# Optimization experiments

Measured on AMD Instinct MI355X. Metric: run time of the kernel, lower is better.

The kernel has to match this reference:

```python
import jax, jax.numpy as jnp
import numpy as np

K_SIM_SCHEDULE = [4, 8, 16]
K_CON_SCHEDULE = [2, 4, 8]
NEG = 1000000000.0


def _dual_adjacency(h, k_sim, k_con):
    """Binary causal dual adjacency (similar / dissimilar), no gradient."""
    B, T, D = h.shape
    h = jax.lax.stop_gradient(h)
    xn = h / jnp.maximum(jnp.linalg.norm(h, axis=-1, keepdims=True), 1e-12)
    sim = jnp.einsum('btd,bsd->bts', xn, xn)                 # (B,T,T)
    past = jnp.tril(jnp.ones((T, T), h.dtype), -1)           # strictly-past mask
    sim = sim * past - NEG * (1.0 - past)
    eff_sim = min(k_sim, T - 1)
    eff_con = min(k_con, max(0, T - 1 - eff_sim))
    bI = jnp.arange(B)[:, None, None]
    tI = jnp.arange(T)[None, :, None]
    A_sim = jnp.zeros((B, T, T), h.dtype)
    if eff_sim > 0:
        _, top_idx = jax.lax.top_k(sim, eff_sim)             # (B,T,k)
        A_sim = A_sim.at[bI, tI, top_idx].set(1.0) * past
    A_con = jnp.zeros((B, T, T), h.dtype)
    if eff_con > 0:
        sim_con = jnp.where(A_sim > 0, NEG, sim)
        _, bot_idx = jax.lax.top_k(-sim_con, eff_con)        # smallest eff_con
        A_con = A_con.at[bI, tI, bot_idx].set(1.0) * past * (1.0 - A_sim)
    return A_sim, A_con


def _aggregate(h, A):
    # unweighted mean over selected neighbors; empty rows -> zeros
    deg = jnp.sum(A, axis=-1, keepdims=True)
    return jnp.einsum('bts,bsd->btd', A, h) / jnp.maximum(deg, 1.0)


def setup_inputs() -> dict:
    key = jax.random.key(0)
    ks = jax.random.split(key, 2)
    B, T, D, R = 4, 2048, 512, 3
    x = jax.random.normal(ks[0], (B, T, D), dtype=jnp.float32)
    gain = jnp.ones((R, D), dtype=jnp.float32)
    bias = jnp.zeros((R, D), dtype=jnp.float32)
    log_mix = jnp.zeros((R,), dtype=jnp.float32)
    log_alpha = jnp.zeros((R,), dtype=jnp.float32)
    log_momentum = jnp.asarray(1.0, dtype=jnp.float32)
    log_scale = jnp.asarray(0.0, dtype=jnp.float32)
    return {"x": x, "gain": gain, "bias": bias, "log_mix": log_mix,
            "log_alpha": log_alpha, "log_momentum": log_momentum,
            "log_scale": log_scale}


def reference(x, gain, bias, log_mix, log_alpha, log_momentum, log_scale):
    momentum = jax.nn.sigmoid(log_momentum)
    scale = jax.nn.softplus(log_scale) + 0.01
    h = x
    for r in range(len(K_SIM_SCHEDULE)):
        mix = jax.nn.sigmoid(log_mix[r])
        alpha = jax.nn.sigmoid(log_alpha[r])
        A_sim, A_con = _dual_adjacency(h, K_SIM_SCHEDULE[r], K_CON_SCHEDULE[r])
        msg_pos = _aggregate(h, A_sim)
        msg_neg = _aggregate(h, A_con)
        ctx = alpha * msg_pos + (1.0 - alpha) * msg_neg
        blended = mix * h + (1.0 - mix) * ctx
        h_new = jax.nn.gelu(blended * gain[r] + bias[r], approximate=False)
        h = momentum * h + (1.0 - momentum) * h_new
    return (h - x) * scale
```

## Files before the change

kernel.cpp:

```cpp
#include <hip/hip_runtime.h>
#include <hip/hip_bf16.h>
#include <cstdint>
#include <cstddef>

#define BB 4
#define TT 2048
#define DD 512
#define NEG_INF (-3.402823466e+38f)
#define POS_INF (3.402823466e+38f)

typedef __attribute__((ext_vector_type(8))) short bf16x8;
typedef __attribute__((ext_vector_type(8))) unsigned short ushort8;
typedef __attribute__((ext_vector_type(4))) float f32x4;

__device__ __forceinline__ float sigmoidf_(float x){ return 1.0f/(1.0f+expf(-x)); }

__device__ __forceinline__ unsigned short f2bf(float x){
  __hip_bfloat16 b = __float2bfloat16(x);
  return *reinterpret_cast<unsigned short*>(&b);
}

__device__ __forceinline__ unsigned int fwd_map(float f){
  unsigned int b = __float_as_uint(f);
  return b ^ ((b & 0x80000000u) ? 0xFFFFFFFFu : 0x80000000u);
}
__device__ __forceinline__ float inv_map(unsigned int u){
  unsigned int b = (u & 0x80000000u) ? (u ^ 0x80000000u) : ~u;
  return __uint_as_float(b);
}

__global__ __launch_bounds__(64) void k_normsplit(const float* __restrict__ h, float* __restrict__ rnorm,
                                                  unsigned short* __restrict__ Xh, unsigned short* __restrict__ Xl){
  int row = blockIdx.x;
  const float* hr = h + (size_t)row*DD;
  int lane = threadIdx.x;
  float4 v0 = *(const float4*)&hr[lane*4];
  float4 v1 = *(const float4*)&hr[lane*4 + 256];
  float ss = v0.x*v0.x+v0.y*v0.y+v0.z*v0.z+v0.w*v0.w
           + v1.x*v1.x+v1.y*v1.y+v1.z*v1.z+v1.w*v1.w;
  #pragma unroll
  for (int off=32; off; off>>=1) ss += __shfl_xor(ss, off);
  float rn = 1.0f / fmaxf(sqrtf(ss), 1e-12f);
  if (lane==0) rnorm[row] = rn;

  float xs[8] = {v0.x,v0.y,v0.z,v0.w,v1.x,v1.y,v1.z,v1.w};
  unsigned short hb[8], lb[8];
  #pragma unroll
  for (int q=0;q<8;q++){
    float xn = xs[q]*rn;
    unsigned short hh = f2bf(xn);
    __hip_bfloat16 bh = *reinterpret_cast<__hip_bfloat16*>(&hh);
    float rem = xn - __bfloat162float(bh);
    hb[q] = hh; lb[q] = f2bf(rem);
  }
  ushort4 h0 = {hb[0],hb[1],hb[2],hb[3]}, h1 = {hb[4],hb[5],hb[6],hb[7]};
  ushort4 l0 = {lb[0],lb[1],lb[2],lb[3]}, l1 = {lb[4],lb[5],lb[6],lb[7]};
  *(ushort4*)&Xh[(size_t)row*DD + lane*4]       = h0;
  *(ushort4*)&Xh[(size_t)row*DD + lane*4 + 256] = h1;
  *(ushort4*)&Xl[(size_t)row*DD + lane*4]       = l0;
  *(ushort4*)&Xl[(size_t)row*DD + lane*4 + 256] = l1;
}

__global__ __launch_bounds__(256) void k_sim(const unsigned short* __restrict__ Xh,
                                             const unsigned short* __restrict__ Xl,
                                             float* __restrict__ sim, int b0){
  int p = blockIdx.x;
  int jt = (int)((sqrtf(8.0f*(float)p + 1.0f) - 1.0f)*0.5f);
  while ((jt+1)*(jt+2)/2 <= p) jt++;
  while (jt*(jt+1)/2 > p) jt--;
  int is = p - jt*(jt+1)/2;

  int bl = blockIdx.y;
  size_t xoff = (size_t)(b0 + bl)*TT*DD;
  const unsigned short* XhB = Xh + xoff;
  const unsigned short* XlB = Xl + xoff;
  float* simb = sim + (size_t)bl*TT*TT;
  int t0 = jt*128, s0 = is*128;

  __shared__ __align__(16) short As[128*32];
  __shared__ __align__(16) short Bs[128*32];

  int tid = threadIdx.x, wave = tid>>6, lane = tid&63;
  int wr = wave>>1, wc = wave&1;

  int srow = tid>>2;
  int sc8  = (tid&3)*8;

  f32x4 acc[4][4];
  #pragma unroll
  for (int m=0;m<4;m++)
    #pragma unroll
    for (int n=0;n<4;n++) acc[m][n] = (f32x4){0.f,0.f,0.f,0.f};

  ushort8 ra0, ra1, rb0, rb1;
  auto gload = [&](int s){
    int pass = s>>4; int kcol = (s&15)*32;
    const unsigned short* sA = (pass<2) ? XhB : XlB;
    const unsigned short* sB = (pass!=1) ? XhB : XlB;
    ra0 = *(const ushort8*)&sA[(size_t)(t0+srow)*DD + kcol + sc8];
    ra1 = *(const ushort8*)&sA[(size_t)(t0+srow+64)*DD + kcol + sc8];
    rb0 = *(const ushort8*)&sB[(size_t)(s0+srow)*DD + kcol + sc8];
    rb1 = *(const ushort8*)&sB[(size_t)(s0+srow+64)*DD + kcol + sc8];
  };

  gload(0);
  for (int s=0; s<48; ++s){
    __syncthreads();
    *(ushort8*)&As[srow*32 + sc8]      = ra0;
    *(ushort8*)&As[(srow+64)*32 + sc8] = ra1;
    *(ushort8*)&Bs[srow*32 + sc8]      = rb0;
    *(ushort8*)&Bs[(srow+64)*32 + sc8] = rb1;
    __syncthreads();
    if (s < 47) gload(s+1);

    int arow = wr*64 + (lane&15);
    int brow = wc*64 + (lane&15);
    int kb = (lane>>4)*8;
    bf16x8 af[4], bf[4];
    #pragma unroll
    for (int m=0;m<4;m++) af[m] = *(const bf16x8*)&As[(arow + m*16)*32 + kb];
    #pragma unroll
    for (int n=0;n<4;n++) bf[n] = *(const bf16x8*)&Bs[(brow + n*16)*32 + kb];
    #pragma unroll
    for (int m=0;m<4;m++)
      #pragma unroll
      for (int n=0;n<4;n++)
        acc[m][n] = __builtin_amdgcn_mfma_f32_16x16x32_bf16(af[m], bf[n], acc[m][n], 0, 0, 0);
  }

  #pragma unroll
  for (int m=0;m<4;m++){
    int t = t0 + wr*64 + m*16 + (lane>>4)*4;
    #pragma unroll
    for (int n=0;n<4;n++){
      int sc = s0 + wc*64 + n*16 + (lane&15);
      float* dst = simb + (size_t)t*TT + sc;
      #pragma unroll
      for (int j=0;j<4;j++) dst[(size_t)j*TT] = acc[m][n][j];
    }
  }
}

#define BMASK 0xFFFFFF00u

__device__ __forceinline__ unsigned int radix24(const float* __restrict__ srow, int t, int k1,
                                                unsigned int flip, int* sh, int lane){
  #pragma unroll
  for (int i=0;i<4;i++) sh[lane + i*64] = 0;
  int t4 = t & ~3;
  for (int s4 = lane*4; s4 < t4; s4 += 256){
    float4 f = *(const float4*)&srow[s4];
    unsigned int u0=fwd_map(f.x)^flip, u1=fwd_map(f.y)^flip, u2=fwd_map(f.z)^flip, u3=fwd_map(f.w)^flip;
    atomicAdd(&sh[u0>>24],1); atomicAdd(&sh[u1>>24],1);
    atomicAdd(&sh[u2>>24],1); atomicAdd(&sh[u3>>24],1);
  }
  for (int s = t4 + lane; s < t; s += 64){
    unsigned int u = fwd_map(srow[s])^flip;
    atomicAdd(&sh[u>>24],1);
  }
  unsigned int pfx = 0u; int kp = k1;
  #pragma unroll
  for (int pass = 0; pass < 3; ++pass){
    int shift = 24 - 8*pass;
    int m4 = sh[4*lane] + sh[4*lane+1] + sh[4*lane+2] + sh[4*lane+3];
    int x = __shfl(m4, 63-lane);
    #pragma unroll
    for (int off = 1; off < 64; off <<= 1){
      int v = __shfl_up(x, off);
      if (lane >= off) x += v;
    }
    int T = __shfl(x, 63-lane);
    int G = T - m4;
    bool hit = (G < kp) && (kp <= T);
    unsigned int npfx = 0u; int nkp = 0;
    if (hit){
      int c = G; int D = 4*lane;
      #pragma unroll
      for (int i = 3; i >= 0; --i){
        int hc = sh[4*lane + i];
        if (kp <= c + hc){ D = 4*lane + i; break; }
        c += hc;
      }
      npfx = pfx | ((unsigned int)D << shift);
      nkp = kp - c;
    }
    unsigned long long hm = __ballot(hit);
    int src = __ffsll(hm) - 1;
    pfx = __shfl(npfx, src);
    kp  = __shfl(nkp, src);
    if (pass == 2) break;

    int nshift = shift - 8;
    unsigned int keep = 0xFFFFFFFFu << shift;
    #pragma unroll
    for (int i=0;i<4;i++) sh[lane + i*64] = 0;
    for (int s4 = lane*4; s4 < t4; s4 += 256){
      float4 f = *(const float4*)&srow[s4];
      unsigned int u0=fwd_map(f.x)^flip, u1=fwd_map(f.y)^flip, u2=fwd_map(f.z)^flip, u3=fwd_map(f.w)^flip;
      if (((u0 ^ pfx) & keep) == 0) atomicAdd(&sh[(u0>>nshift)&255],1);
      if (((u1 ^ pfx) & keep) == 0) atomicAdd(&sh[(u1>>nshift)&255],1);
      if (((u2 ^ pfx) & keep) == 0) atomicAdd(&sh[(u2>>nshift)&255],1);
      if (((u3 ^ pfx) & keep) == 0) atomicAdd(&sh[(u3>>nshift)&255],1);
    }
    for (int s = t4 + lane; s < t; s += 64){
      unsigned int u = fwd_map(srow[s])^flip;
      if (((u ^ pfx) & keep) == 0) atomicAdd(&sh[(u>>nshift)&255],1);
    }
  }
  return pfx;
}

template<int ESIM, int ECON>
__global__ __launch_bounds__(256) void k_topk(const float* __restrict__ sim, int b0,
                                              const float* __restrict__ h, const float* __restrict__ rnorm,
                                              int* __restrict__ topidx, int* __restrict__ botidx,
                                              int* __restrict__ bcnt){
  constexpr int K1  = ESIM + 8;
  constexpr int K1B = ESIM + ECON + 8;
  constexpr int CANDCAP = 40;
  constexpr int EQCAP = 44;
  constexpr float TAU = 5e-5f;
  __shared__ int s_hist[4][256];
  __shared__ int s_cand[4][CANDCAP];
  __shared__ int s_eq[4][EQCAP];
  __shared__ int s_sel[4][ESIM];
  __shared__ int s_bot[4][16];
  __shared__ int s_cnt[4][2];

  int tid = threadIdx.x, lane = tid & 63, wid = tid >> 6;
  int lrow = blockIdx.x*4 + wid;
  int bl = lrow >> 11, t = lrow & (TT-1);
  int gb = b0 + bl;
  int grow = (gb << 11) | t;

  if (t <= ESIM){
    if (lane < t) topidx[(size_t)grow*16 + lane] = lane;
    if (lane == 0) bcnt[grow] = 0;
    return;
  }
  const float* srow = sim + (size_t)lrow*TT;
  const float* hb  = h + (size_t)gb*TT*DD;
  const float* rnb = rnorm + (size_t)gb*TT;

  int* sh    = s_hist[wid];
  int* scand = s_cand[wid];
  int* seq   = s_eq[wid];
  int* ssel  = s_sel[wid];
  int* sbot  = s_bot[wid];

  int k1 = min(t, K1);
  unsigned int thr = radix24(srow, t, k1, 0u, sh, lane);

  if (lane == 0){ s_cnt[wid][0] = 0; s_cnt[wid][1] = 0; }
  int t4 = t & ~3;
  for (int s4 = lane*4; s4 < t4; s4 += 256){
    float4 f = *(const float4*)&srow[s4];
    unsigned int uu[4] = {fwd_map(f.x), fwd_map(f.y), fwd_map(f.z), fwd_map(f.w)};
    #pragma unroll
    for (int q=0;q<4;q++){
      unsigned int b24 = uu[q] & BMASK;
      if (b24 > thr){ int p = atomicAdd(&s_cnt[wid][0],1); if (p < CANDCAP) scand[p] = s4+q; }
      else if (b24 == thr){ int p = atomicAdd(&s_cnt[wid][1],1); if (p < EQCAP) seq[p] = s4+q; }
    }
  }
  for (int s = t4 + lane; s < t; s += 64){
    unsigned int b24 = fwd_map(srow[s]) & BMASK;
    if (b24 > thr){ int p = atomicAdd(&s_cnt[wid][0],1); if (p < CANDCAP) scand[p] = s; }
    else if (b24 == thr){ int p = atomicAdd(&s_cnt[wid][1],1); if (p < EQCAP) seq[p] = s; }
  }
  int c_gt = min(s_cnt[wid][0], CANDCAP);
  int c_eq = min(s_cnt[wid][1], EQCAP);
  int ncand = min(c_gt + c_eq, 64);

  unsigned int myu = 0u; int myi = 0x7fffffff;
  if (lane < ncand){
    myi = (lane < c_gt) ? scand[lane] : seq[lane - c_gt];
    myu = fwd_map(srow[myi]);
  }

  float vA = 0.f, vB = 0.f;
  {
    unsigned int cu = myu; int ci = myi;
    #pragma unroll
    for (int k = 0; k <= ESIM; ++k){
      unsigned int bu = cu; int bi = ci;
      #pragma unroll
      for (int off=32; off; off>>=1){
        unsigned int ou = __shfl_xor(bu, off); int oi = __shfl_xor(bi, off);
        if (ou > bu || (ou == bu && oi < bi)){ bu = ou; bi = oi; }
      }
      if (k < ESIM && lane == 0) ssel[k] = bi;
      if (k == ESIM-1) vA = inv_map(bu);
      if (k == ESIM)   vB = inv_map(bu);
      if (ci == bi){ cu = 0u; ci = 0x7fffffff; }
    }
  }

  bool resc = (vA - vB < TAU);
  if (resc){
    const float* hq = hb + (size_t)t*DD;
    float rt = rnb[t];
    float4 q0 = *(const float4*)&hq[lane*4];
    float4 q1 = *(const float4*)&hq[lane*4 + 256];
    float ev = NEG_INF;
    for (int j = 0; j < ncand; ++j){
      int idx = (j < c_gt) ? scand[j] : seq[j - c_gt];
      const float* hc = hb + (size_t)idx*DD;
      float4 c0 = *(const float4*)&hc[lane*4];
      float4 c1 = *(const float4*)&hc[lane*4 + 256];
      float pp = q0.x*c0.x+q0.y*c0.y+q0.z*c0.z+q0.w*c0.w
               + q1.x*c1.x+q1.y*c1.y+q1.z*c1.z+q1.w*c1.w;
      #pragma unroll
      for (int off=32; off; off>>=1) pp += __shfl_xor(pp, off);
      float ex = pp * rt * rnb[idx];
      if (lane == j) ev = ex;
    }
    float rv = (lane < ncand) ? ev : NEG_INF;
    int   ri = myi;
    #pragma unroll
    for (int k = 0; k < ESIM; ++k){
      float bv = rv; int bi = ri;
      #pragma unroll
      for (int off=32; off; off>>=1){
        float ov = __shfl_xor(bv, off); int oi = __shfl_xor(bi, off);
        if (ov > bv || (ov == bv && oi < bi)){ bv = ov; bi = oi; }
      }
      if (lane == 0) ssel[k] = bi;
      if (ri == bi) rv = NEG_INF;
    }
  }
  if (lane < ESIM) topidx[(size_t)grow*16 + lane] = ssel[lane];

  int need = ECON - (TT - t);
  int cnt = 0;
  if (need > 0){
    constexpr unsigned int FLIP = 0xFFFFFFFFu;
    int k1b = min(t, K1B);
    unsigned int thrb = radix24(srow, t, k1b, FLIP, sh, lane);

    if (lane == 0){ s_cnt[wid][0] = 0; s_cnt[wid][1] = 0; }
    for (int s4 = lane*4; s4 < t4; s4 += 256){
      float4 f = *(const float4*)&srow[s4];
      unsigned int uu[4] = {fwd_map(f.x)^FLIP, fwd_map(f.y)^FLIP, fwd_map(f.z)^FLIP, fwd_map(f.w)^FLIP};
      #pragma unroll
      for (int q=0;q<4;q++){
        unsigned int b24 = uu[q] & BMASK;
        if (b24 > thrb){ int p = atomicAdd(&s_cnt[wid][0],1); if (p < CANDCAP) scand[p] = s4+q; }
        else if (b24 == thrb){ int p = atomicAdd(&s_cnt[wid][1],1); if (p < EQCAP) seq[p] = s4+q; }
      }
    }
    for (int s = t4 + lane; s < t; s += 64){
      unsigned int u = fwd_map(srow[s])^FLIP;
      unsigned int b24 = u & BMASK;
      if (b24 > thrb){ int p = atomicAdd(&s_cnt[wid][0],1); if (p < CANDCAP) scand[p] = s; }
      else if (b24 == thrb){ int p = atomicAdd(&s_cnt[wid][1],1); if (p < EQCAP) seq[p] = s; }
    }
    int bc_gt = min(s_cnt[wid][0], CANDCAP);
    int bc_eq = min(s_cnt[wid][1], EQCAP);
    int ncb = min(bc_gt + bc_eq, 64);

    unsigned int mu = 0u; int mi = 0x7fffffff;
    if (lane < ncb){
      mi = (lane < bc_gt) ? scand[lane] : seq[lane - bc_gt];
      mu = fwd_map(srow[mi]) ^ FLIP;
    }
    float wA = 0.f, wB = 0.f;
    unsigned int cu = mu; int ci = mi;
    #pragma unroll
    for (int k = 0; k < K1B; ++k){
      if (k < ncb && cnt < need + 8){
        unsigned int bu = cu; int bi = ci;
        #pragma unroll
        for (int off=32; off; off>>=1){
          unsigned int ou = __shfl_xor(bu, off); int oi = __shfl_xor(bi, off);
          if (ou > bu || (ou == bu && oi < bi)){ bu = ou; bi = oi; }
        }
        if (ci == bi){ cu = 0u; ci = 0x7fffffff; }
        bool mem = false;
        #pragma unroll
        for (int j=0;j<ESIM;j++) if (ssel[j] == bi) mem = true;
        if (!mem){
          if (lane == 0) sbot[cnt] = bi;
          float val = inv_map(bu ^ FLIP);
          if (cnt == need-1) wA = val;
          if (cnt == need)   wB = val;
          cnt++;
        }
      }
    }
    int npick = min(need, cnt);
    bool rb = (cnt > need) && (wB - wA < TAU);
    if (!rb){
      if (lane < npick) botidx[(size_t)grow*8 + lane] = sbot[lane];
    } else {
      const float* hq = hb + (size_t)t*DD;
      float rt = rnb[t];
      float4 q0 = *(const float4*)&hq[lane*4];
      float4 q1 = *(const float4*)&hq[lane*4 + 256];
      float ev = POS_INF; int ei = 0x7fffffff;
      for (int j = 0; j < cnt; ++j){
        int idx = sbot[j];
        const float* hc = hb + (size_t)idx*DD;
        float4 c0 = *(const float4*)&hc[lane*4];
        float4 c1 = *(const float4*)&hc[lane*4 + 256];
        float pp = q0.x*c0.x+q0.y*c0.y+q0.z*c0.z+q0.w*c0.w
                 + q1.x*c1.x+q1.y*c1.y+q1.z*c1.z+q1.w*c1.w;
        #pragma unroll
        for (int off=32; off; off>>=1) pp += __shfl_xor(pp, off);
        float ex = pp * rt * rnb[idx];
        if (lane == j){ ev = ex; ei = idx; }
      }
      #pragma unroll
      for (int k = 0; k < ECON; ++k){
        if (k < npick){
          float bv = ev; int bi = ei;
          #pragma unroll
          for (int off=32; off; off>>=1){
            float ov = __shfl_xor(bv, off); int oi = __shfl_xor(bi, off);
            if (ov < bv || (ov == bv && oi < bi)){ bv = ov; bi = oi; }
          }
          if (lane == 0) botidx[(size_t)grow*8 + k] = bi;
          if (ei == bi) ev = POS_INF;
        }
      }
    }
    cnt = npick;
  }
  if (lane == 0) bcnt[grow] = cnt;
}

__global__ __launch_bounds__(256) void k_agg(const float* __restrict__ hsrc, float* __restrict__ hdst,
                                             const int* __restrict__ topidx, const int* __restrict__ botidx,
                                             const int* __restrict__ bcnt,
                                             const float* __restrict__ gain, const float* __restrict__ bias,
                                             const float* __restrict__ log_mix, const float* __restrict__ log_alpha,
                                             const float* __restrict__ log_momentum, int r, int eff_sim){
  int row = blockIdx.x;
  int b = row >> 11; int t = row & (TT-1);
  int n_sim = min(eff_sim, t);
  int n_con = bcnt[row];
  float mix      = sigmoidf_(log_mix[r]);
  float alpha    = sigmoidf_(log_alpha[r]);
  float momentum = sigmoidf_(log_momentum[0]);
  const float* hb = hsrc + (size_t)b*TT*DD;

  __shared__ int sidx[16];
  __shared__ int scidx[8];
  if (threadIdx.x < 16) sidx[threadIdx.x]  = (threadIdx.x < n_sim) ? topidx[(size_t)row*16 + threadIdx.x] : 0;
  if (threadIdx.x < 8)  scidx[threadIdx.x] = (threadIdx.x < n_con) ? botidx[(size_t)row*8  + threadIdx.x] : 0;
  __syncthreads();

  #pragma unroll
  for (int e = threadIdx.x; e < DD; e += 256){
    float sp = 0.f;
    for (int j=0;j<n_sim;j++) sp += hb[(size_t)sidx[j]*DD + e];
    float sn = 0.f;
    for (int j=0;j<n_con;j++) sn += hb[(size_t)scidx[j]*DD + e];
    float mp = sp / (float)max(n_sim, 1);
    float mn = sn / (float)max(n_con, 1);
    float ctx = alpha*mp + (1.f-alpha)*mn;
    float hv = hsrc[(size_t)row*DD + e];
    float blended = mix*hv + (1.f-mix)*ctx;
    float u = blended*gain[e] + bias[e];
    float g = 0.5f*u*(1.0f + erff(u*0.7071067811865475f));
    hdst[(size_t)row*DD + e] = momentum*hv + (1.f-momentum)*g;
  }
}

__global__ __launch_bounds__(256) void k_final(const float* __restrict__ hfin, const float* __restrict__ x,
                                               const float* __restrict__ log_scale, float* __restrict__ out, int n){
  float scale = log1pf(expf(log_scale[0])) + 0.01f;
  int i = blockIdx.x*256 + threadIdx.x;
  if (i < n) out[i] = (hfin[i] - x[i]) * scale;
}

extern "C" void kernel_launch(void* const* d_in, const int* in_sizes, int n_in,
                              void* d_out, int out_size, void* d_ws, size_t ws_size,
                              hipStream_t stream) {
  const float* x         = (const float*)d_in[0];
  const float* gain      = (const float*)d_in[1];
  const float* bias      = (const float*)d_in[2];
  const float* log_mix   = (const float*)d_in[3];
  const float* log_alpha = (const float*)d_in[4];
  const float* log_mom   = (const float*)d_in[5];
  const float* log_scale = (const float*)d_in[6];

  float* hA = (float*)d_out;
  char* ws = (char*)d_ws;
  size_t off = 0;
  auto alloc = [&](size_t bytes){ void* p = ws + off; off += (bytes + 255) & ~(size_t)255; return p; };

  float*          hB     = (float*)alloc((size_t)BB*TT*DD*4);
  float*          rnorm  = (float*)alloc((size_t)BB*TT*4);
  int*            topidx = (int*)  alloc((size_t)BB*TT*16*4);
  int*            botidx = (int*)  alloc((size_t)BB*TT*8*4);
  int*            bcnt   = (int*)  alloc((size_t)BB*TT*4);
  unsigned short* Xh     = (unsigned short*)alloc((size_t)BB*TT*DD*2);
  unsigned short* Xl     = (unsigned short*)alloc((size_t)BB*TT*DD*2);

  size_t rem = (ws_size > off) ? (ws_size - off) : 0;
  int cb = (int)(rem / ((size_t)TT*TT*4));
  if (cb < 1) cb = 1;
  if (cb > BB) cb = BB;
  float* sim = (float*)alloc((size_t)cb*TT*TT*4);

  const float* hsrc = x;
  float* hdst = hB;
  const int ks[3] = {4, 8, 16};

  for (int r = 0; r < 3; ++r){
    k_normsplit<<<BB*TT, 64, 0, stream>>>(hsrc, rnorm, Xh, Xl);
    for (int b0 = 0; b0 < BB; b0 += cb){
      int nb = (BB - b0 < cb) ? (BB - b0) : cb;
      dim3 g(136, nb);
      k_sim<<<g, 256, 0, stream>>>(Xh, Xl, sim, b0);
      if (r == 0)      k_topk<4,2><<<nb*TT/4, 256, 0, stream>>>(sim, b0, hsrc, rnorm, topidx, botidx, bcnt);
      else if (r == 1) k_topk<8,4><<<nb*TT/4, 256, 0, stream>>>(sim, b0, hsrc, rnorm, topidx, botidx, bcnt);
      else             k_topk<16,8><<<nb*TT/4, 256, 0, stream>>>(sim, b0, hsrc, rnorm, topidx, botidx, bcnt);
    }
    k_agg<<<BB*TT, 256, 0, stream>>>(hsrc, hdst, topidx, botidx, bcnt,
                                     gain + (size_t)r*DD, bias + (size_t)r*DD,
                                     log_mix, log_alpha, log_mom, r, ks[r]);
    if (r == 0){ hsrc = hB; hdst = hA; }
    else if (r == 1){ hsrc = hA; hdst = hB; }
  }
  k_final<<<(BB*TT*DD)/256, 256, 0, stream>>>(hB, x, log_scale, (float*)d_out, BB*TT*DD);
}
```

Baseline: 472.4 us.

## Add per-lane register top-4 fast path for similarity top-k selection

```diff
diff --git a/kernel.cpp b/kernel.cpp
--- a/kernel.cpp
+++ b/kernel.cpp
@@ -27,6 +27,12 @@
 __device__ __forceinline__ float inv_map(unsigned int u){
   unsigned int b = (u & 0x80000000u) ? (u ^ 0x80000000u) : ~u;
   return __uint_as_float(b);
+}
+
+__device__ __forceinline__ unsigned long long shfl_xor64(unsigned long long x, int off){
+  unsigned int hi = __shfl_xor((unsigned int)(x >> 32), off);
+  unsigned int lo = __shfl_xor((unsigned int)x, off);
+  return ((unsigned long long)hi << 32) | lo;
 }
 
 __global__ __launch_bounds__(64) void k_normsplit(const float* __restrict__ h, float* __restrict__ rnorm,
@@ -247,92 +253,145 @@
   int* seq   = s_eq[wid];
   int* ssel  = s_sel[wid];
   int* sbot  = s_bot[wid];
-
-  int k1 = min(t, K1);
-  unsigned int thr = radix24(srow, t, k1, 0u, sh, lane);
-
-  if (lane == 0){ s_cnt[wid][0] = 0; s_cnt[wid][1] = 0; }
   int t4 = t & ~3;
+
+  unsigned long long kv0=0, kv1=0, kv2=0, kv3=0;
+  {
+    #define MKKEY(F,S) ((((unsigned long long)fwd_map(F)) << 32) | (unsigned int)(~(S)))
+    #define INS(KK) do{ unsigned long long a=(KK); \
+      if (a > kv3){ \
+        if (a > kv0){ unsigned long long tq=kv0; kv0=a; a=tq; } \
+        if (a > kv1){ unsigned long long tq=kv1; kv1=a; a=tq; } \
+        if (a > kv2){ unsigned long long tq=kv2; kv2=a; a=tq; } \
+        kv3=a; } }while(0)
+    for (int s4 = lane*4; s4 < t4; s4 += 256){
+      float4 f = *(const float4*)&srow[s4];
+      INS(MKKEY(f.x,s4)); INS(MKKEY(f.y,s4+1)); INS(MKKEY(f.z,s4+2)); INS(MKKEY(f.w,s4+3));
+    }
+    for (int s = t4 + lane; s < t; s += 64) INS(MKKEY(srow[s],s));
+  }
+
+  int myidx = 0x7fffffff;
+  float vA = 0.f, vB = 0.f;
+  unsigned long long keyLast = 0ull;
+  #pragma unroll
+  for (int k = 0; k <= ESIM; ++k){
+    unsigned long long bk = kv0;
+    #pragma unroll
+    for (int off=32; off; off>>=1){
+      unsigned long long ok = shfl_xor64(bk, off);
+      if (ok > bk) bk = ok;
+    }
+    if (kv0 == bk){ kv0=kv1; kv1=kv2; kv2=kv3; kv3=0ull; }
+    if (lane == k) myidx = (int)(~(unsigned int)bk);
+    if (k == ESIM-1) vA = inv_map((unsigned int)(bk >> 32));
+    if (k == ESIM){ vB = inv_map((unsigned int)(bk >> 32)); keyLast = bk; }
+  }
+
+  int cnt = 0;
   for (int s4 = lane*4; s4 < t4; s4 += 256){
     float4 f = *(const float4*)&srow[s4];
-    unsigned int uu[4] = {fwd_map(f.x), fwd_map(f.y), fwd_map(f.z), fwd_map(f.w)};
-    #pragma unroll
-    for (int q=0;q<4;q++){
-      unsigned int b24 = uu[q] & BMASK;
-      if (b24 > thr){ int p = atomicAdd(&s_cnt[wid][0],1); if (p < CANDCAP) scand[p] = s4+q; }
-      else if (b24 == thr){ int p = atomicAdd(&s_cnt[wid][1],1); if (p < EQCAP) seq[p] = s4+q; }
-    }
-  }
-  for (int s = t4 + lane; s < t; s += 64){
-    unsigned int b24 = fwd_map(srow[s]) & BMASK;
-    if (b24 > thr){ int p = atomicAdd(&s_cnt[wid][0],1); if (p < CANDCAP) scand[p] = s; }
-    else if (b24 == thr){ int p = atomicAdd(&s_cnt[wid][1],1); if (p < EQCAP) seq[p] = s; }
-  }
-  int c_gt = min(s_cnt[wid][0], CANDCAP);
-  int c_eq = min(s_cnt[wid][1], EQCAP);
-  int ncand = min(c_gt + c_eq, 64);
-
-  unsigned int myu = 0u; int myi = 0x7fffffff;
-  if (lane < ncand){
-    myi = (lane < c_gt) ? scand[lane] : seq[lane - c_gt];
-    myu = fwd_map(srow[myi]);
-  }
-
-  float vA = 0.f, vB = 0.f;
-  {
-    unsigned int cu = myu; int ci = myi;
-    #pragma unroll
-    for (int k = 0; k <= ESIM; ++k){
-      unsigned int bu = cu; int bi = ci;
-      #pragma unroll
-      for (int off=32; off; off>>=1){
-        unsigned int ou = __shfl_xor(bu, off); int oi = __shfl_xor(bi, off);
-        if (ou > bu || (ou == bu && oi < bi)){ bu = ou; bi = oi; }
-      }
-      if (k < ESIM && lane == 0) ssel[k] = bi;
-      if (k == ESIM-1) vA = inv_map(bu);
-      if (k == ESIM)   vB = inv_map(bu);
-      if (ci == bi){ cu = 0u; ci = 0x7fffffff; }
-    }
-  }
-
-  bool resc = (vA - vB < TAU);
-  if (resc){
-    const float* hq = hb + (size_t)t*DD;
-    float rt = rnb[t];
-    float4 q0 = *(const float4*)&hq[lane*4];
-    float4 q1 = *(const float4*)&hq[lane*4 + 256];
-    float ev = NEG_INF;
-    for (int j = 0; j < ncand; ++j){
-      int idx = (j < c_gt) ? scand[j] : seq[j - c_gt];
-      const float* hc = hb + (size_t)idx*DD;
-      float4 c0 = *(const float4*)&hc[lane*4];
-      float4 c1 = *(const float4*)&hc[lane*4 + 256];
-      float pp = q0.x*c0.x+q0.y*c0.y+q0.z*c0.z+q0.w*c0.w
-               + q1.x*c1.x+q1.y*c1.y+q1.z*c1.z+q1.w*c1.w;
-      #pragma unroll
-      for (int off=32; off; off>>=1) pp += __shfl_xor(pp, off);
-      float ex = pp * rt * rnb[idx];
-      if (lane == j) ev = ex;
-    }
-    float rv = (lane < ncand) ? ev : NEG_INF;
-    int   ri = myi;
-    #pragma unroll
-    for (int k = 0; k < ESIM; ++k){
-      float bv = rv; int bi = ri;
-      #pragma unroll
-      for (int off=32; off; off>>=1){
-        float ov = __shfl_xor(bv, off); int oi = __shfl_xor(bi, off);
-        if (ov > bv || (ov == bv && oi < bi)){ bv = ov; bi = oi; }
-      }
-      if (lane == 0) ssel[k] = bi;
-      if (ri == bi) rv = NEG_INF;
-    }
-  }
-  if (lane < ESIM) topidx[(size_t)grow*16 + lane] = ssel[lane];
+    cnt += (MKKEY(f.x,s4)   > keyLast);
+    cnt += (MKKEY(f.y,s4+1) > keyLast);
+    cnt += (MKKEY(f.z,s4+2) > keyLast);
+    cnt += (MKKEY(f.w,s4+3) > keyLast);
+  }
+  for (int s = t4 + lane; s < t; s += 64) cnt += (MKKEY(srow[s],s) > keyLast);
+  #pragma unroll
+  for (int off=32; off; off>>=1) cnt += __shfl_xor(cnt, off);
+
+  bool fb = (cnt != ESIM) || (vA - vB < TAU);
+  if (!fb){
+    if (lane < ESIM){
+      ssel[lane] = myidx;
+      topidx[(size_t)grow*16 + lane] = myidx;
+    }
+  } else {
+    int k1 = min(t, K1);
+    unsigned int thr = radix24(srow, t, k1, 0u, sh, lane);
+
+    if (lane == 0){ s_cnt[wid][0] = 0; s_cnt[wid][1] = 0; }
+    for (int s4 = lane*4; s4 < t4; s4 += 256){
+      float4 f = *(const float4*)&srow[s4];
+      unsigned int uu[4] = {fwd_map(f.x), fwd_map(f.y), fwd_map(f.z), fwd_map(f.w)};
+      #pragma unroll
+      for (int q=0;q<4;q++){
+        unsigned int b24 = uu[q] & BMASK;
+        if (b24 > thr){ int p = atomicAdd(&s_cnt[wid][0],1); if (p < CANDCAP) scand[p] = s4+q; }
+        else if (b24 == thr){ int p = atomicAdd(&s_cnt[wid][1],1); if (p < EQCAP) seq[p] = s4+q; }
+      }
+    }
+    for (int s = t4 + lane; s < t; s += 64){
+      unsigned int b24 = fwd_map(srow[s]) & BMASK;
+      if (b24 > thr){ int p = atomicAdd(&s_cnt[wid][0],1); if (p < CANDCAP) scand[p] = s; }
+      else if (b24 == thr){ int p = atomicAdd(&s_cnt[wid][1],1); if (p < EQCAP) seq[p] = s; }
+    }
+    int c_gt = min(s_cnt[wid][0], CANDCAP);
+    int c_eq = min(s_cnt[wid][1], EQCAP);
+    int ncand = min(c_gt + c_eq, 64);
+
+    unsigned int myu = 0u; int myi = 0x7fffffff;
+    if (lane < ncand){
+      myi = (lane < c_gt) ? scand[lane] : seq[lane - c_gt];
+      myu = fwd_map(srow[myi]);
+    }
+
+    float fvA = 0.f, fvB = 0.f;
+    {
+      unsigned int cu = myu; int ci = myi;
+      #pragma unroll
+      for (int k = 0; k <= ESIM; ++k){
+        unsigned int bu = cu; int bi = ci;
+        #pragma unroll
+        for (int off=32; off; off>>=1){
+          unsigned int ou = __shfl_xor(bu, off); int oi = __shfl_xor(bi, off);
+          if (ou > bu || (ou == bu && oi < bi)){ bu = ou; bi = oi; }
+        }
+        if (k < ESIM && lane == 0) ssel[k] = bi;
+        if (k == ESIM-1) fvA = inv_map(bu);
+        if (k == ESIM)   fvB = inv_map(bu);
+        if (ci == bi){ cu = 0u; ci = 0x7fffffff; }
+      }
+    }
+
+    bool resc = (fvA - fvB < TAU);
+    if (resc){
+      const float* hq = hb + (size_t)t*DD;
+      float rt = rnb[t];
+      float4 q0 = *(const float4*)&hq[lane*4];
+      float4 q1 = *(const float4*)&hq[lane*4 + 256];
+      float ev = NEG_INF;
+      for (int j = 0; j < ncand; ++j){
+        int idx = (j < c_gt) ? scand[j] : seq[j - c_gt];
+        const float* hc = hb + (size_t)idx*DD;
+        float4 c0 = *(const float4*)&hc[lane*4];
+        float4 c1 = *(const float4*)&hc[lane*4 + 256];
+        float pp = q0.x*c0.x+q0.y*c0.y+q0.z*c0.z+q0.w*c0.w
+                 + q1.x*c1.x+q1.y*c1.y+q1.z*c1.z+q1.w*c1.w;
+        #pragma unroll
+        for (int off=32; off; off>>=1) pp += __shfl_xor(pp, off);
+        float ex = pp * rt * rnb[idx];
+        if (lane == j) ev = ex;
+      }
+      float rv = (lane < ncand) ? ev : NEG_INF;
+      int   ri = myi;
+      #pragma unroll
+      for (int k = 0; k < ESIM; ++k){
+        float bv = rv; int bi = ri;
+        #pragma unroll
+        for (int off=32; off; off>>=1){
+          float ov = __shfl_xor(bv, off); int oi = __shfl_xor(bi, off);
+          if (ov > bv || (ov == bv && oi < bi)){ bv = ov; bi = oi; }
+        }
+        if (lane == 0) ssel[k] = bi;
+        if (ri == bi) rv = NEG_INF;
+      }
+    }
+    if (lane < ESIM) topidx[(size_t)grow*16 + lane] = ssel[lane];
+  }
 
   int need = ECON - (TT - t);
-  int cnt = 0;
+  int cnt2 = 0;
   if (need > 0){
     constexpr unsigned int FLIP = 0xFFFFFFFFu;
     int k1b = min(t, K1B);
@@ -368,7 +427,7 @@
     unsigned int cu = mu; int ci = mi;
     #pragma unroll
     for (int k = 0; k < K1B; ++k){
-      if (k < ncb && cnt < need + 8){
+      if (k < ncb && cnt2 < need + 8){
         unsigned int bu = cu; int bi = ci;
         #pragma unroll
         for (int off=32; off; off>>=1){
@@ -380,16 +439,16 @@
         #pragma unroll
         for (int j=0;j<ESIM;j++) if (ssel[j] == bi) mem = true;
         if (!mem){
-          if (lane == 0) sbot[cnt] = bi;
+          if (lane == 0) sbot[cnt2] = bi;
           float val = inv_map(bu ^ FLIP);
-          if (cnt == need-1) wA = val;
-          if (cnt == need)   wB = val;
-          cnt++;
+          if (cnt2 == need-1) wA = val;
+          if (cnt2 == need)   wB = val;
+          cnt2++;
         }
       }
     }
-    int npick = min(need, cnt);
-    bool rb = (cnt > need) && (wB - wA < TAU);
+    int npick = min(need, cnt2);
+    bool rb = (cnt2 > need) && (wB - wA < TAU);
     if (!rb){
       if (lane < npick) botidx[(size_t)grow*8 + lane] = sbot[lane];
     } else {
@@ -398,7 +457,7 @@
       float4 q0 = *(const float4*)&hq[lane*4];
       float4 q1 = *(const float4*)&hq[lane*4 + 256];
       float ev = POS_INF; int ei = 0x7fffffff;
-      for (int j = 0; j < cnt; ++j){
+      for (int j = 0; j < cnt2; ++j){
         int idx = sbot[j];
         const float* hc = hb + (size_t)idx*DD;
         float4 c0 = *(const float4*)&hc[lane*4];
@@ -424,9 +483,9 @@
         }
       }
     }
-    cnt = npick;
-  }
-  if (lane == 0) bcnt[grow] = cnt;
+    cnt2 = npick;
+  }
+  if (lane == 0) bcnt[grow] = cnt2;
 }
 
 __global__ __launch_bounds__(256) void k_agg(const float* __restrict__ hsrc, float* __restrict__ hdst,
```

New measurement: 462.9 us. 2.0% less time.
